# Performance work log

Measured on AMD Instinct MI355X. Metric: run time of the kernel, lower is better.

The kernel has to match this reference:

```python
import jax, jax.numpy as jnp
import numpy as np


def _gather_masked(seq, mask, k):
    """Order-preserving gather of the k True positions per row (apply_mask).
    mask rows are constructed to have exactly k ones, so pad_sequence is a no-op."""
    # stable argsort of ~mask puts True-position indices first, in original order
    idx = jnp.argsort(jnp.logical_not(mask), axis=1, stable=True)[:, :k]  # (B, k)
    return jnp.take_along_axis(seq, idx[:, :, None], axis=1)  # (B, k, H)


def setup_inputs() -> dict:
    B, L, H, K = 8, 4096, 1024, 512
    key = jax.random.key(0)
    k1, k2, k3 = jax.random.split(key, 3)
    sequence_output = jax.random.normal(k1, (B, L, H), dtype=jnp.float32)
    # masks: exactly K source and K target positions per sample (disjoint)
    rng = np.random.default_rng(0)
    src_mask = np.zeros((B, L), dtype=bool)
    tgt_mask = np.zeros((B, L), dtype=bool)
    for i in range(B):
        perm = rng.permutation(L)
        src_mask[i, perm[:K]] = True
        tgt_mask[i, perm[K:2 * K]] = True
    weight = jax.random.normal(k2, (2 * H,), dtype=jnp.float32) * 0.02  # classifier Linear(2H -> 1)
    bias = jax.random.normal(k3, (1,), dtype=jnp.float32) * 0.02
    return {
        "sequence_output": sequence_output,
        "source_mask": jnp.asarray(src_mask),
        "target_mask": jnp.asarray(tgt_mask),
        "weight": weight,
        "bias": bias,
        "num_tokens": K,
    }


def reference(sequence_output, source_mask, target_mask, weight, bias, num_tokens):
    B, L, H = sequence_output.shape
    K = num_tokens  # S == T == K (required by the original expand())
    src = _gather_masked(sequence_output, source_mask, K)  # (B, K, H)
    tgt = _gather_masked(sequence_output, target_mask, K)  # (B, K, H)
    # Original: cat([src.unsqueeze(2).expand(B,S,T,H), tgt.unsqueeze(2).expand(B,S,T,H)])
    # -> combined[b,s,t] = [src[b,s], tgt[b,s]]  (target indexed by s, faithful to source)
    # Decompose Linear(2H,1) on the broadcast-concat: col[b,s] = src@w1 + tgt@w2 + b,
    # then broadcast over t. Same math, no (B,S,T,2H) intermediate.
    col = src @ weight[:H] + tgt @ weight[H:] + bias[0]  # (B, K)
    return jnp.broadcast_to(col[:, :, None], (B, K, K))  # logits (B, S, T)
```

## Files before the change

kernel.cpp:

```cpp
#include <hip/hip_runtime.h>
#include <hip/hip_bf16.h>


#define L_DIM 4096
#define H_DIM 1024
#define K_DIM 512
#define B_DIM 8
#define PACKED_K (K_DIM | (K_DIM << 16))

typedef float f32x4 __attribute__((ext_vector_type(4)));

__device__ __forceinline__ unsigned nib4(unsigned w) {
    unsigned x = w | (w >> 4); x |= x >> 2; x |= x >> 1; x &= 0x01010101u;
    return ((x * 0x01020408u) >> 24) & 0xFu;
}
__device__ __forceinline__ unsigned mask16b(uint4 u) {
    return nib4(u.x) | (nib4(u.y) << 4) | (nib4(u.z) << 8) | (nib4(u.w) << 12);
}
__device__ __forceinline__ int nth16(unsigned m, int n) {
    int pos = 0, c;
    c = __popc(m & 0xFFu); if (n >= c) { n -= c; pos += 8; m >>= 8; }
    c = __popc(m & 0xFu);  if (n >= c) { n -= c; pos += 4; m >>= 4; }
    c = __popc(m & 0x3u);  if (n >= c) { n -= c; pos += 2; m >>= 2; }
    c = (int)(m & 1u);     if (n >= c) { pos += 1; }
    return pos;
}

__global__ __launch_bounds__(256) void fused_kernel(
    const float* __restrict__ seq,
    const void* __restrict__ smask, const void* __restrict__ tmask,
    const float* __restrict__ weight, const float* __restrict__ bias,
    float* __restrict__ out)
{
    const int tid  = threadIdx.x;
    const int wid  = tid >> 6;
    const int lane = tid & 63;
    const int bb   = blockIdx.x;
    const int b    = bb >> 7;
    const int sg   = (bb & 127) << 2;

    __shared__ int wtot[4];
    __shared__ int posLds[8];

    const uint4* sb = (const uint4*)((const unsigned char*)smask + (size_t)b * L_DIM);
    const uint4* tb = (const uint4*)((const unsigned char*)tmask + (size_t)b * L_DIM);
    unsigned mS = mask16b(sb[tid]);
    unsigned mT = mask16b(tb[tid]);
    int packed = __popc(mS) | (__popc(mT) << 16);

    int x = packed;
#pragma unroll
    for (int off = 1; off < 64; off <<= 1) {
        int y = __shfl_up(x, off, 64);
        if (lane >= off) x += y;
    }
    if (lane == 63) wtot[wid] = x;
    __syncthreads();
    int off_ = 0, tot = 0;
#pragma unroll
    for (int w = 0; w < 4; ++w) { int v = wtot[w]; tot += v; if (w < wid) off_ += v; }
    x += off_;

    if (tot != PACKED_K) {
        __syncthreads();
        const uint4* si = (const uint4*)((const unsigned*)smask + (size_t)b * L_DIM) + tid * 4;
        const uint4* ti = (const uint4*)((const unsigned*)tmask + (size_t)b * L_DIM) + tid * 4;
        mS = 0u; mT = 0u;
#pragma unroll
        for (int j = 0; j < 4; ++j) {
            uint4 u = si[j], v = ti[j];
            const int base = j * 4;
            mS |= (((u.x != 0) ? 1u : 0u) << base) | (((u.y != 0) ? 1u : 0u) << (base + 1))
                | (((u.z != 0) ? 1u : 0u) << (base + 2)) | (((u.w != 0) ? 1u : 0u) << (base + 3));
            mT |= (((v.x != 0) ? 1u : 0u) << base) | (((v.y != 0) ? 1u : 0u) << (base + 1))
                | (((v.z != 0) ? 1u : 0u) << (base + 2)) | (((v.w != 0) ? 1u : 0u) << (base + 3));
        }
        packed = __popc(mS) | (__popc(mT) << 16);
        x = packed;
#pragma unroll
        for (int off = 1; off < 64; off <<= 1) {
            int y = __shfl_up(x, off, 64);
            if (lane >= off) x += y;
        }
        if (lane == 63) wtot[wid] = x;
        __syncthreads();
        off_ = 0;
#pragma unroll
        for (int w = 0; w < 4; ++w) { int v = wtot[w]; if (w < wid) off_ += v; }
        x += off_;
    }

    const int exc  = x - packed;
    const int excS = exc & 0xffff, excT = exc >> 16;
    const int cntS = __popc(mS), cntT = __popc(mT);
#pragma unroll
    for (int j = 0; j < 4; ++j) {
        const int s = sg + j;
        if (s >= excS && s < excS + cntS) posLds[j]     = tid * 16 + nth16(mS, s - excS);
        if (s >= excT && s < excT + cntT) posLds[4 + j] = tid * 16 + nth16(mT, s - excT);
    }
    __syncthreads();

    const int ps = posLds[wid];
    const int pt = posLds[4 + wid];

    const float4* __restrict__ srow = (const float4*)(seq + ((size_t)b * L_DIM + ps) * H_DIM);
    const float4* __restrict__ trow = (const float4*)(seq + ((size_t)b * L_DIM + pt) * H_DIM);
    const float4* __restrict__ w1 = (const float4*)(weight);
    const float4* __restrict__ w2 = (const float4*)(weight + H_DIM);

    float acc0 = 0.f, acc1 = 0.f;
#pragma unroll
    for (int j = 0; j < 4; ++j) {
        const int i = lane + 64 * j;
        float4 a = srow[i], wa = w1[i];
        float4 c = trow[i], wc = w2[i];
        acc0 += a.x * wa.x + a.y * wa.y + a.z * wa.z + a.w * wa.w;
        acc1 += c.x * wc.x + c.y * wc.y + c.z * wc.z + c.w * wc.w;
    }
    float acc = acc0 + acc1;
#pragma unroll
    for (int off = 32; off; off >>= 1) acc += __shfl_xor(acc, off, 64);

    const float col = acc + bias[0];
    const f32x4 v = {col, col, col, col};
    f32x4* orow = (f32x4*)(out + ((size_t)(b * K_DIM + sg + wid)) * K_DIM);
    __builtin_nontemporal_store(v, &orow[lane]);
    __builtin_nontemporal_store(v, &orow[lane + 64]);
}

extern "C" void kernel_launch(void* const* d_in, const int* in_sizes, int n_in,
                              void* d_out, int out_size, void* d_ws, size_t ws_size,
                              hipStream_t stream) {
    const float* seq    = (const float*)d_in[0];
    const void*  smask  = d_in[1];
    const void*  tmask  = d_in[2];
    const float* weight = (const float*)d_in[3];
    const float* bias   = (const float*)d_in[4];
    float* out = (float*)d_out;
    (void)d_ws; (void)ws_size;

    fused_kernel<<<1024, 256, 0, stream>>>(seq, smask, tmask, weight, bias, out);
}
```

Measured before the change: 13.49 us.

## Split each output row across two waves and double the grid

```diff
diff --git a/kernel.cpp b/kernel.cpp
--- a/kernel.cpp
+++ b/kernel.cpp
@@ -36,11 +36,14 @@
     const int wid  = tid >> 6;
     const int lane = tid & 63;
     const int bb   = blockIdx.x;
-    const int b    = bb >> 7;
-    const int sg   = (bb & 127) << 2;
+    const int b    = bb >> 8;
+    const int sg   = (bb & 255) << 1;
+    const int p    = wid >> 1;
+    const int r    = wid & 1;
 
     __shared__ int wtot[4];
-    __shared__ int posLds[8];
+    __shared__ int posLds[4];
+    __shared__ float part[4];
 
     const uint4* sb = (const uint4*)((const unsigned char*)smask + (size_t)b * L_DIM);
     const uint4* tb = (const uint4*)((const unsigned char*)tmask + (size_t)b * L_DIM);
@@ -94,39 +97,34 @@
     const int excS = exc & 0xffff, excT = exc >> 16;
     const int cntS = __popc(mS), cntT = __popc(mT);
 #pragma unroll
-    for (int j = 0; j < 4; ++j) {
+    for (int j = 0; j < 2; ++j) {
         const int s = sg + j;
         if (s >= excS && s < excS + cntS) posLds[j]     = tid * 16 + nth16(mS, s - excS);
-        if (s >= excT && s < excT + cntT) posLds[4 + j] = tid * 16 + nth16(mT, s - excT);
+        if (s >= excT && s < excT + cntT) posLds[2 + j] = tid * 16 + nth16(mT, s - excT);
     }
     __syncthreads();
 
-    const int ps = posLds[wid];
-    const int pt = posLds[4 + wid];
+    const int pos = posLds[r * 2 + p];
+    const float4* __restrict__ row = (const float4*)(seq + ((size_t)b * L_DIM + pos) * H_DIM);
+    const float4* __restrict__ wv  = (const float4*)(weight + r * H_DIM);
 
-    const float4* __restrict__ srow = (const float4*)(seq + ((size_t)b * L_DIM + ps) * H_DIM);
-    const float4* __restrict__ trow = (const float4*)(seq + ((size_t)b * L_DIM + pt) * H_DIM);
-    const float4* __restrict__ w1 = (const float4*)(weight);
-    const float4* __restrict__ w2 = (const float4*)(weight + H_DIM);
-
-    float acc0 = 0.f, acc1 = 0.f;
+    float acc = 0.f;
 #pragma unroll
     for (int j = 0; j < 4; ++j) {
         const int i = lane + 64 * j;
-        float4 a = srow[i], wa = w1[i];
-        float4 c = trow[i], wc = w2[i];
-        acc0 += a.x * wa.x + a.y * wa.y + a.z * wa.z + a.w * wa.w;
-        acc1 += c.x * wc.x + c.y * wc.y + c.z * wc.z + c.w * wc.w;
+        float4 a = row[i], wa = wv[i];
+        acc += a.x * wa.x + a.y * wa.y + a.z * wa.z + a.w * wa.w;
     }
-    float acc = acc0 + acc1;
 #pragma unroll
     for (int off = 32; off; off >>= 1) acc += __shfl_xor(acc, off, 64);
 
-    const float col = acc + bias[0];
+    if (lane == 0) part[wid] = acc;
+    __syncthreads();
+
+    const float col = part[2 * p] + part[2 * p + 1] + bias[0];
     const f32x4 v = {col, col, col, col};
-    f32x4* orow = (f32x4*)(out + ((size_t)(b * K_DIM + sg + wid)) * K_DIM);
-    __builtin_nontemporal_store(v, &orow[lane]);
-    __builtin_nontemporal_store(v, &orow[lane + 64]);
+    f32x4* orow = (f32x4*)(out + ((size_t)(b * K_DIM + sg + p)) * K_DIM);
+    orow[r * 64 + lane] = v;
 }
 
 extern "C" void kernel_launch(void* const* d_in, const int* in_sizes, int n_in,
@@ -140,5 +138,5 @@
     float* out = (float*)d_out;
     (void)d_ws; (void)ws_size;
 
-    fused_kernel<<<1024, 256, 0, stream>>>(seq, smask, tmask, weight, bias, out);
+    fused_kernel<<<2048, 256, 0, stream>>>(seq, smask, tmask, weight, bias, out);
 }
```

Result: slower. 15.92 us (+17.9%).
